# Performance work log

Measured on AMD Instinct MI355X. Metric: run time of the kernel, lower is better.

Reference implementation:

```python
import jax, jax.numpy as jnp
import numpy as np

N_WORD = 50000
N_DOC = 10000
E_WW = 800000
E_WD = 320000


def _sage(h_src, h_dst, src, dst, n_dst, W_self, W_neigh, b):
    # DGL SAGEConv('mean'): fc_self(h_dst) + fc_neigh(mean_{u in N(v)} h_u) + bias
    ones = jnp.ones((src.shape[0],), dtype=h_src.dtype)
    deg = jax.ops.segment_sum(ones, dst, num_segments=n_dst)            # [n_dst]
    agg = jax.ops.segment_sum(h_src[src], dst, num_segments=n_dst)      # [n_dst, d]
    mean = agg / jnp.maximum(deg, 1.0)[:, None]                          # zero for isolated
    return h_dst @ W_self + mean @ W_neigh + b


def _layer(xw, xd, edges, Ws, Wn, b):
    (ww_s, ww_d, wwr_s, wwr_d, wd_s, wd_d, wdr_s, wdr_d) = edges
    # relations targeting 'word': word2word, word2wordr, word2documentr
    h_ww = _sage(xw, xw, ww_s, ww_d, N_WORD, Ws[0], Wn[0], b[0])
    h_wwr = _sage(xw, xw, wwr_s, wwr_d, N_WORD, Ws[1], Wn[1], b[1])
    h_wdr = _sage(xd, xw, wdr_s, wdr_d, N_WORD, Ws[3], Wn[3], b[3])
    # relation targeting 'document': word2document
    h_wd = _sage(xw, xd, wd_s, wd_d, N_DOC, Ws[2], Wn[2], b[2])
    # HeteroGraphConv aggregate='stack' then torch.sum(dim=1) == sum over relations; then relu
    return jax.nn.relu(h_ww + h_wwr + h_wdr), jax.nn.relu(h_wd)


def setup_inputs() -> dict:
    key = jax.random.key(0)
    ks = jax.random.split(key, 20)
    d_in, d_h = 256, 128
    inp = {
        "x_word": jax.random.normal(ks[0], (N_WORD, d_in), jnp.float32),
        "x_doc": jax.random.normal(ks[1], (N_DOC, d_in), jnp.float32),
        "ww_src": jax.random.randint(ks[2], (E_WW,), 0, N_WORD, jnp.int32),
        "ww_dst": jax.random.randint(ks[3], (E_WW,), 0, N_WORD, jnp.int32),
        "wwr_src": jax.random.randint(ks[4], (E_WW,), 0, N_WORD, jnp.int32),
        "wwr_dst": jax.random.randint(ks[5], (E_WW,), 0, N_WORD, jnp.int32),
        "wd_src": jax.random.randint(ks[6], (E_WD,), 0, N_WORD, jnp.int32),
        "wd_dst": jax.random.randint(ks[7], (E_WD,), 0, N_DOC, jnp.int32),
        "wdr_src": jax.random.randint(ks[8], (E_WD,), 0, N_DOC, jnp.int32),
        "wdr_dst": jax.random.randint(ks[9], (E_WD,), 0, N_WORD, jnp.int32),
        "Wself1": jax.random.normal(ks[10], (4, d_in, d_h), jnp.float32) * (1.0 / np.sqrt(d_in)),
        "Wneigh1": jax.random.normal(ks[11], (4, d_in, d_h), jnp.float32) * (1.0 / np.sqrt(d_in)),
        "b1": jnp.zeros((4, d_h), jnp.float32),
        "Wself2": jax.random.normal(ks[12], (4, d_h, d_h), jnp.float32) * (1.0 / np.sqrt(d_h)),
        "Wneigh2": jax.random.normal(ks[13], (4, d_h, d_h), jnp.float32) * (1.0 / np.sqrt(d_h)),
        "b2": jnp.zeros((4, d_h), jnp.float32),
        "lin_w": jax.random.normal(ks[14], (1, d_h), jnp.float32) * (1.0 / np.sqrt(d_h)),
        "lin_b": jnp.ones((1,), jnp.float32),
    }
    return inp


def reference(x_word, x_doc, ww_src, ww_dst, wwr_src, wwr_dst, wd_src, wd_dst,
              wdr_src, wdr_dst, Wself1, Wneigh1, b1, Wself2, Wneigh2, b2, lin_w, lin_b):
    edges = (ww_src, ww_dst, wwr_src, wwr_dst, wd_src, wd_dst, wdr_src, wdr_dst)
    xw, xd = _layer(x_word, x_doc, edges, Wself1, Wneigh1, b1)
    xw, xd = _layer(xw, xd, edges, Wself2, Wneigh2, b2)
    out_w = jax.nn.sigmoid(xw @ lin_w.T + lin_b)  # [N_WORD, 1]
    out_d = jax.nn.sigmoid(xd @ lin_w.T + lin_b)  # [N_DOC, 1]
    return out_w, out_d
```

## Files before the change

### kernel.cpp

```cpp
#include <hip/hip_runtime.h>
#include <math.h>

#define N_WORD 50000
#define N_DOC  10000
#define E_WW   800000
#define E_WD   320000
#define D_IN   256
#define D_H    128

#define NPB    256
#define NBK_W  196
#define NBK_D  40
#define BKT    (3 * NBK_W + NBK_D)
#define EPB    8192
#define NBLK_WW 98
#define NBLK_WD 40
#define NBLK_TOT (2 * NBLK_WW + 2 * NBLK_WD)
#define PACK_BLKS 145

#define CAP_WW  4736
#define CAP_WDR 2176
#define CAP_WD  8960

#define WSTRIP ((N_WORD + 63) / 64)
#define DSTRIP ((N_DOC + 63) / 64)
#define NSTRIP (WSTRIP + DSTRIP)

typedef __attribute__((ext_vector_type(8))) short short8;
typedef __attribute__((ext_vector_type(4))) float f32x4;
typedef __attribute__((ext_vector_type(2))) float f32x2;

__device__ inline unsigned short f2bf(float f) {
  unsigned u = __float_as_uint(f);
  u = (u + 0x7fffu + ((u >> 16) & 1u)) >> 16;
  return (unsigned short)u;
}

__device__ inline float bflo(unsigned u) { return __uint_as_float(u << 16); }
__device__ inline float bfhi(unsigned u) { return __uint_as_float(u & 0xffff0000u); }

struct G6 { const short* B[6]; unsigned short* C[6]; };

#define BCH 16384

template <int ABF, int K>
__device__ void gemm_body(const void* __restrict__ Aw, const void* __restrict__ Ad,
                          const G6& g, int blk, short* __restrict__ Bs) {
  constexpr int KT = K >> 5;
  constexpr int NCH = KT / 4;
  int tid = threadIdx.x;
  int wid = tid >> 6, lane = tid & 63;
  const void* A; int M, row0, h0, h1;
  if (blk < WSTRIP) { A = Aw; M = N_WORD; row0 = blk << 6; h0 = 0; h1 = 4; }
  else { A = Ad; M = N_DOC; row0 = (blk - WSTRIP) << 6; h0 = 4; h1 = 6; }
  int r = lane & 15, quad = lane >> 4;
  int m0 = row0 + wid * 16;
  int mA = m0 + r; if (mA >= M) mA = M - 1;
  short8 afr[KT];
  if (ABF) {
    const short* ap = (const short*)A + (size_t)mA * K + quad * 8;
#pragma unroll
    for (int kt = 0; kt < KT; ++kt) afr[kt] = *(const short8*)(ap + kt * 32);
  } else {
    const float* ap = (const float*)A + (size_t)mA * K + quad * 8;
#pragma unroll
    for (int kt = 0; kt < KT; ++kt) {
      float4 a0 = *(const float4*)(ap + kt * 32);
      float4 a1 = *(const float4*)(ap + kt * 32 + 4);
      short8 v;
      v[0] = (short)f2bf(a0.x); v[1] = (short)f2bf(a0.y);
      v[2] = (short)f2bf(a0.z); v[3] = (short)f2bf(a0.w);
      v[4] = (short)f2bf(a1.x); v[5] = (short)f2bf(a1.y);
      v[6] = (short)f2bf(a1.z); v[7] = (short)f2bf(a1.w);
      afr[kt] = v;
    }
  }
  for (int h = h0; h < h1; ++h) {
    const short* Bp = g.B[h];
    f32x4 acc[8];
#pragma unroll
    for (int nt = 0; nt < 8; ++nt) acc[nt] = (f32x4){0.f, 0.f, 0.f, 0.f};
    for (int c = 0; c < NCH; ++c) {
      const short* src = Bp + (size_t)c * BCH;
#pragma unroll
      for (int i = 0; i < 8; ++i) {
        int o = (i * 256 + tid) * 8;
        *(short8*)(Bs + o) = *(const short8*)(src + o);
      }
      __syncthreads();
#pragma unroll
      for (int ktl = 0; ktl < 4; ++ktl) {
        const short* bbase = Bs + ktl * 4096 + lane * 8;
#pragma unroll
        for (int nt = 0; nt < 8; ++nt) {
          short8 bf = *(const short8*)(bbase + nt * 512);
          acc[nt] = __builtin_amdgcn_mfma_f32_16x16x32_bf16(afr[c * 4 + ktl], bf, acc[nt], 0, 0, 0);
        }
      }
      __syncthreads();
    }
    unsigned short* C = g.C[h];
#pragma unroll
    for (int nt = 0; nt < 8; ++nt)
#pragma unroll
      for (int rr = 0; rr < 4; ++rr) {
        int row = m0 + quad * 4 + rr;
        if (row < M) C[(size_t)row * 128 + nt * 16 + r] = f2bf(acc[nt][rr]);
      }
  }
}

__global__ __launch_bounds__(256, 2) void gemm2_kernel(
    const void* __restrict__ Aw, const void* __restrict__ Ad, G6 g) {
  __shared__ short Bs[BCH];
  gemm_body<1, 128>(Aw, Ad, g, blockIdx.x, Bs);
}

__global__ __launch_bounds__(256) void prep_kernel(
    const float* __restrict__ Ws1, const float* __restrict__ Wn1,
    const float* __restrict__ Ws2, const float* __restrict__ Wn2,
    short* __restrict__ Bp1, short* __restrict__ Bp2,
    const float* __restrict__ b1, const float* __restrict__ b2,
    float* __restrict__ bs1, float* __restrict__ bs2, int* __restrict__ bcnt,
    unsigned* __restrict__ zA, unsigned* __restrict__ zB,
    unsigned* __restrict__ zC, unsigned* __restrict__ zD) {
  int b = blockIdx.x;
  if (b == PACK_BLKS) {
    for (int i = threadIdx.x; i < BKT; i += 256) bcnt[i] = 0;
    if (threadIdx.x < 64) {
      zA[(size_t)N_WORD * 64 + threadIdx.x] = 0;
      zB[(size_t)N_WORD * 64 + threadIdx.x] = 0;
      zC[(size_t)N_WORD * 64 + threadIdx.x] = 0;
      zD[(size_t)N_DOC * 64 + threadIdx.x] = 0;
    }
    return;
  }
  int tid = b * 256 + threadIdx.x;
  const int L1T = 6 * 4096;
  const int L2T = 6 * 2048;
  if (tid >= L1T + L2T) {
    int t = tid - (L1T + L2T);
    if (t < 128) bs1[t] = b1[t] + b1[128 + t] + b1[384 + t];
    else if (t < 256) { int u = t - 128; bs2[u] = b2[u] + b2[128 + u] + b2[384 + u]; }
    return;
  }
  const float *src0, *src1 = nullptr, *src2 = nullptr;
  short* dstp;
  int kt, nt, lane;
  if (tid < L1T) {
    int mat = tid / 4096, rem = tid % 4096;
    kt = rem / 512; nt = (rem / 64) % 8; lane = rem % 64;
    const int W1 = 256 * 128;
    if (mat == 0) { src0 = Ws1; src1 = Ws1 + W1; src2 = Ws1 + 3 * W1; }
    else if (mat <= 4) src0 = Wn1 + (size_t)(mat - 1) * W1;
    else src0 = Ws1 + 2 * W1;
    dstp = Bp1 + (size_t)mat * W1 + ((size_t)(kt * 8 + nt) * 64 + lane) * 8;
  } else {
    int t2 = tid - L1T;
    int mat = t2 / 2048, rem = t2 % 2048;
    kt = rem / 512; nt = (rem / 64) % 8; lane = rem % 64;
    const int W2 = 128 * 128;
    if (mat == 0) { src0 = Ws2; src1 = Ws2 + W2; src2 = Ws2 + 3 * W2; }
    else if (mat <= 4) src0 = Wn2 + (size_t)(mat - 1) * W2;
    else src0 = Ws2 + 2 * W2;
    dstp = Bp2 + (size_t)mat * W2 + ((size_t)(kt * 8 + nt) * 64 + lane) * 8;
  }
  int n = nt * 16 + (lane & 15);
  int kb = kt * 32 + (lane >> 4) * 8;
  short8 v;
#pragma unroll
  for (int j = 0; j < 8; ++j) {
    float f = src0[(size_t)(kb + j) * 128 + n];
    if (src1) f += src1[(size_t)(kb + j) * 128 + n] + src2[(size_t)(kb + j) * 128 + n];
    v[j] = (short)f2bf(f);
  }
  *(short8*)dstp = v;
}

__device__ inline void rel_map(int b, const int* wwd, const int* wwrd, const int* wdrd,
                               const int* wdd, const int*& dst, int& E, int& gbase, int& lb) {
  if (b < NBLK_WW) { dst = wwd; E = E_WW; gbase = 0; lb = b; }
  else if (b < 2 * NBLK_WW) { dst = wwrd; E = E_WW; gbase = NBK_W; lb = b - NBLK_WW; }
  else if (b < 2 * NBLK_WW + NBLK_WD) { dst = wdrd; E = E_WD; gbase = 2 * NBK_W; lb = b - 2 * NBLK_WW; }
  else { dst = wdd; E = E_WD; gbase = 3 * NBK_W; lb = b - 2 * NBLK_WW - NBLK_WD; }
}

struct BinLDS {
  unsigned buf[EPB];
  int hist[NBK_W];
  int lofs[NBK_W];
  int gofs[NBK_W];
  int lcur[NBK_W];
  int sm[256];
};

union FusedLDS {
  BinLDS bin;
  short bs[BCH];
};

__global__ __launch_bounds__(256, 4) void bin_gemm1(
    const int* wws, const int* wwd, const int* wwrs, const int* wwrd,
    const int* wdrs, const int* wdrd, const int* wds, const int* wdd,
    int* bcnt, unsigned* st_ww, unsigned* st_wwr, unsigned* st_wdr, unsigned* st_wd,
    const float* __restrict__ Aw, const float* __restrict__ Ad, G6 g) {
  __shared__ FusedLDS U;
  int b = blockIdx.x;
  if (b >= NBLK_TOT) {
    gemm_body<0, 256>(Aw, Ad, g, b - NBLK_TOT, U.bs);
    return;
  }
  BinLDS& L = U.bin;
  const int* dst; int E, gbase, lb;
  rel_map(b, wwd, wwrd, wdrd, wdd, dst, E, gbase, lb);
  const int* src; unsigned* st; int cap;
  if (b < NBLK_WW) { src = wws; st = st_ww; cap = CAP_WW; }
  else if (b < 2 * NBLK_WW) { src = wwrs; st = st_wwr; cap = CAP_WW; }
  else if (b < 2 * NBLK_WW + NBLK_WD) { src = wdrs; st = st_wdr; cap = CAP_WDR; }
  else { src = wds; st = st_wd; cap = CAP_WD; }
  int tid = threadIdx.x;
  int e0 = lb * EPB;
  int ecnt = E - e0; if (ecnt > EPB) ecnt = EPB;
  if (tid < NBK_W) L.hist[tid] = 0;
  __syncthreads();
  int dcache[EPB / 256];
#pragma unroll
  for (int k = 0; k < EPB / 256; ++k) {
    int i = e0 + k * 256 + tid;
    int d = (i < E) ? dst[i] : -1;
    dcache[k] = d;
    if (d >= 0) atomicAdd(&L.hist[d >> 8], 1);
  }
  __syncthreads();
  {
    int v = (tid < NBK_W) ? L.hist[tid] : 0;
    L.sm[tid] = v;
    __syncthreads();
    for (int o = 1; o < 256; o <<= 1) {
      int add = (tid >= o) ? L.sm[tid - o] : 0;
      __syncthreads();
      L.sm[tid] += add;
      __syncthreads();
    }
    if (tid < NBK_W) {
      int ex = L.sm[tid] - v;
      L.lofs[tid] = ex;
      L.lcur[tid] = ex;
      int base = v ? atomicAdd(&bcnt[gbase + tid], v) : 0;
      L.gofs[tid] = (int)((size_t)tid * cap) + base - ex;
    }
  }
  __syncthreads();
#pragma unroll
  for (int k = 0; k < EPB / 256; ++k) {
    int d = dcache[k];
    if (d >= 0) {
      int i = e0 + k * 256 + tid;
      int bk = d >> 8;
      int p = atomicAdd(&L.lcur[bk], 1);
      L.buf[p] = ((unsigned)bk << 24) | ((unsigned)(d & 255) << 16) |
                 (unsigned)(src[i] & 0xFFFF);
    }
  }
  __syncthreads();
#pragma unroll
  for (int k = 0; k < EPB / 256; ++k) {
    int p = k * 256 + tid;
    if (p < ecnt) {
      unsigned e = L.buf[p];
      st[L.gofs[e >> 24] + p] = e & 0x00FFFFFFu;
    }
  }
}

struct CSRB {
  const unsigned *st_ww, *st_wwr, *st_wdr, *st_wd;
  unsigned short *c_ww, *c_wwr, *c_wdr, *c_wd;
  int *rp_ww, *rp_wwr, *rp_wdr, *rp_wd;
  const int* bcnt;
};

__global__ __launch_bounds__(256) void place_kernel(CSRB q) {
  __shared__ int cnt[256], off[256], sm[256];
  int g = blockIdx.x;
  const unsigned* st; unsigned short* csr; int* rp; int relFirst, relLast, n, cap, Etot;
  if (g < NBK_W)            { st = q.st_ww;  csr = q.c_ww;  rp = q.rp_ww;  relFirst = 0;         relLast = NBK_W - 1;     n = N_WORD; cap = CAP_WW;  Etot = E_WW; }
  else if (g < 2 * NBK_W)   { st = q.st_wwr; csr = q.c_wwr; rp = q.rp_wwr; relFirst = NBK_W;     relLast = 2 * NBK_W - 1; n = N_WORD; cap = CAP_WW;  Etot = E_WW; }
  else if (g < 3 * NBK_W)   { st = q.st_wdr; csr = q.c_wdr; rp = q.rp_wdr; relFirst = 2 * NBK_W; relLast = 3 * NBK_W - 1; n = N_WORD; cap = CAP_WDR; Etot = E_WD; }
  else                      { st = q.st_wd;  csr = q.c_wd;  rp = q.rp_wd;  relFirst = 3 * NBK_W; relLast = BKT - 1;       n = N_DOC;  cap = CAP_WD;  Etot = E_WD; }
  int cb = g - relFirst;
  int tid = threadIdx.x;
  int v = (tid < cb) ? q.bcnt[relFirst + tid] : 0;
  sm[tid] = v;
  __syncthreads();
  for (int o = 128; o > 0; o >>= 1) {
    if (tid < o) sm[tid] += sm[tid + o];
    __syncthreads();
  }
  int bstart = sm[0];
  if (g == relLast && tid == 0) rp[n] = Etot;
  __syncthreads();
  int node_base = cb << 8;
  int node_cnt = n - node_base; if (node_cnt > NPB) node_cnt = NPB;
  int ecnt = q.bcnt[g];
  const unsigned* w = st + (size_t)cb * cap;
  cnt[tid] = 0;
  __syncthreads();
  for (int j = tid; j < ecnt; j += 256) atomicAdd(&cnt[w[j] >> 16], 1);
  __syncthreads();
  int c = cnt[tid];
  sm[tid] = c;
  __syncthreads();
  for (int o = 1; o < 256; o <<= 1) {
    int add = (tid >= o) ? sm[tid - o] : 0;
    __syncthreads();
    sm[tid] += add;
    __syncthreads();
  }
  int ex = sm[tid] - c;
  off[tid] = ex;
  if (tid < node_cnt) rp[node_base + tid] = bstart + ex;
  __syncthreads();
  for (int j = tid; j < ecnt; j += 256) {
    unsigned e = w[j];
    int p = atomicAdd(&off[e >> 16], 1);
    csr[bstart + p] = (unsigned short)(e & 0xFFFFu);
  }
}

__device__ inline void accum_rel4(const uint4* __restrict__ Y,
                                  const unsigned short* __restrict__ csr,
                                  int beg, int end, int lane, int r, int g,
                                  int zrow, f32x2* __restrict__ f) {
  int deg = end - beg;
  if (deg <= 0) return;
  f32x2 a0 = {0.f, 0.f}, a1 = a0, a2 = a0, a3 = a0;
  for (int base = beg; base < end; base += 64) {
    int cnt = end - base; if (cnt > 64) cnt = 64;
    int ld = base + lane;
    int idx = (ld < end) ? (int)csr[ld] : zrow;
    for (int j = 0; j < cnt; j += 16) {
      uint4 u[4];
#pragma unroll
      for (int t = 0; t < 4; ++t) {
        int sv = __shfl(idx, j + (t << 2) + g, 64);
        u[t] = Y[(unsigned)((sv << 4) + r)];
      }
#pragma unroll
      for (int t = 0; t < 4; ++t) {
        a0 += (f32x2){bflo(u[t].x), bfhi(u[t].x)};
        a1 += (f32x2){bflo(u[t].y), bfhi(u[t].y)};
        a2 += (f32x2){bflo(u[t].z), bfhi(u[t].z)};
        a3 += (f32x2){bflo(u[t].w), bfhi(u[t].w)};
      }
    }
  }
  float inv = 1.0f / (float)deg;
  f[0] += a0 * inv; f[1] += a1 * inv; f[2] += a2 * inv; f[3] += a3 * inv;
}

__global__ __launch_bounds__(256) void gather_all(
    const unsigned* __restrict__ y_ww, const unsigned* __restrict__ y_wwr,
    const unsigned* __restrict__ y_wdr, const unsigned* __restrict__ y_wd,
    const unsigned short* __restrict__ c_ww, const unsigned short* __restrict__ c_wwr,
    const unsigned short* __restrict__ c_wdr, const unsigned short* __restrict__ c_wd,
    const int* __restrict__ r_ww, const int* __restrict__ r_wwr,
    const int* __restrict__ r_wdr, const int* __restrict__ r_wd,
    const unsigned* __restrict__ tW, const unsigned* __restrict__ tD,
    const float* __restrict__ bW, const float* __restrict__ bD,
    const float* __restrict__ lw, const float* __restrict__ lb,
    unsigned* __restrict__ oW16, unsigned* __restrict__ oD16,
    float* __restrict__ oF, int mode) {
  int gn = (blockIdx.x << 2) + (threadIdx.x >> 6);
  if (gn >= N_WORD + N_DOC) return;
  int lane = threadIdx.x & 63;
  int r = lane & 15, g = lane >> 4;
  f32x2 f[4];
#pragma unroll
  for (int i = 0; i < 4; ++i) f[i] = (f32x2){0.f, 0.f};
  bool isw = (gn < N_WORD);
  int node = isw ? gn : gn - N_WORD;
  if (isw) {
    accum_rel4((const uint4*)y_ww, c_ww, r_ww[node], r_ww[node + 1], lane, r, g, N_WORD, f);
    accum_rel4((const uint4*)y_wwr, c_wwr, r_wwr[node], r_wwr[node + 1], lane, r, g, N_WORD, f);
    accum_rel4((const uint4*)y_wdr, c_wdr, r_wdr[node], r_wdr[node + 1], lane, r, g, N_DOC, f);
  } else {
    accum_rel4((const uint4*)y_wd, c_wd, r_wd[node], r_wd[node + 1], lane, r, g, N_WORD, f);
  }
#pragma unroll
  for (int i = 0; i < 4; ++i) {
    f[i].x += __shfl_xor(f[i].x, 16, 64);
    f[i].y += __shfl_xor(f[i].y, 16, 64);
    f[i].x += __shfl_xor(f[i].x, 32, 64);
    f[i].y += __shfl_xor(f[i].y, 32, 64);
  }
  const unsigned* tS = isw ? tW : tD;
  uint4 tu = ((const uint4*)tS)[(unsigned)((node << 4) + r)];
  const float* bs = isw ? bW : bD;
  float4 bv0 = ((const float4*)bs)[2 * r];
  float4 bv1 = ((const float4*)bs)[2 * r + 1];
  f[0].x = fmaxf(f[0].x + bflo(tu.x) + bv0.x, 0.f);
  f[0].y = fmaxf(f[0].y + bfhi(tu.x) + bv0.y, 0.f);
  f[1].x = fmaxf(f[1].x + bflo(tu.y) + bv0.z, 0.f);
  f[1].y = fmaxf(f[1].y + bfhi(tu.y) + bv0.w, 0.f);
  f[2].x = fmaxf(f[2].x + bflo(tu.z) + bv1.x, 0.f);
  f[2].y = fmaxf(f[2].y + bfhi(tu.z) + bv1.y, 0.f);
  f[3].x = fmaxf(f[3].x + bflo(tu.w) + bv1.z, 0.f);
  f[3].y = fmaxf(f[3].y + bfhi(tu.w) + bv1.w, 0.f);
  if (mode == 1) {
    if (g == 0) {
      uint4 pk;
      pk.x = (unsigned)f2bf(f[0].x) | ((unsigned)f2bf(f[0].y) << 16);
      pk.y = (unsigned)f2bf(f[1].x) | ((unsigned)f2bf(f[1].y) << 16);
      pk.z = (unsigned)f2bf(f[2].x) | ((unsigned)f2bf(f[2].y) << 16);
      pk.w = (unsigned)f2bf(f[3].x) | ((unsigned)f2bf(f[3].y) << 16);
      unsigned* o = isw ? oW16 : oD16;
      ((uint4*)o)[(unsigned)((node << 4) + r)] = pk;
    }
  } else {
    float4 lv0 = ((const float4*)lw)[2 * r];
    float4 lv1 = ((const float4*)lw)[2 * r + 1];
    float s = f[0].x * lv0.x + f[0].y * lv0.y + f[1].x * lv0.z + f[1].y * lv0.w +
              f[2].x * lv1.x + f[2].y * lv1.y + f[3].x * lv1.z + f[3].y * lv1.w;
#pragma unroll
    for (int off = 8; off > 0; off >>= 1) s += __shfl_xor(s, off, 64);
    if (lane == 0) oF[isw ? node : N_WORD + node] = 1.0f / (1.0f + expf(-(s + lb[0])));
  }
}

extern "C" void kernel_launch(void* const* d_in, const int* in_sizes, int n_in,
                              void* d_out, int out_size, void* d_ws, size_t ws_size,
                              hipStream_t stream) {
  const float* xw      = (const float*)d_in[0];
  const float* xd      = (const float*)d_in[1];
  const int*   ww_src  = (const int*)d_in[2];
  const int*   ww_dst  = (const int*)d_in[3];
  const int*   wwr_src = (const int*)d_in[4];
  const int*   wwr_dst = (const int*)d_in[5];
  const int*   wd_src  = (const int*)d_in[6];
  const int*   wd_dst  = (const int*)d_in[7];
  const int*   wdr_src = (const int*)d_in[8];
  const int*   wdr_dst = (const int*)d_in[9];
  const float* Ws1     = (const float*)d_in[10];
  const float* Wn1     = (const float*)d_in[11];
  const float* b1      = (const float*)d_in[12];
  const float* Ws2     = (const float*)d_in[13];
  const float* Wn2     = (const float*)d_in[14];
  const float* b2      = (const float*)d_in[15];
  const float* lin_w   = (const float*)d_in[16];
  const float* lin_b   = (const float*)d_in[17];
  float* out = (float*)d_out;

  char* p = (char*)d_ws;
  auto alloc = [&](size_t nbytes) {
    char* r = p;
    p += (nbytes + 255) & ~(size_t)255;
    return r;
  };
  unsigned* twA  = (unsigned*)alloc((size_t)N_WORD * D_H * 2);
  unsigned* tdA  = (unsigned*)alloc((size_t)N_DOC * D_H * 2);
  unsigned* xw1B = (unsigned*)alloc((size_t)N_WORD * D_H * 2 + 256);
  unsigned* xd1B = (unsigned*)alloc((size_t)N_DOC * D_H * 2);
  unsigned* yB0 = (unsigned*)alloc((size_t)N_WORD * D_H * 2);
  unsigned* yB1 = (unsigned*)alloc(((size_t)NBK_W * CAP_WDR + (size_t)NBK_D * CAP_WD) * 4);
  unsigned* yB2 = (unsigned*)alloc((size_t)N_WORD * D_H * 2 + 256);
  unsigned* ydB = (unsigned*)alloc((size_t)N_DOC * D_H * 2 + 256);
  unsigned short* csr_ww  = (unsigned short*)alloc((size_t)E_WW * 2);
  unsigned short* csr_wwr = (unsigned short*)alloc((size_t)E_WW * 2);
  unsigned short* csr_wdr = (unsigned short*)alloc((size_t)E_WD * 2);
  unsigned short* csr_wd  = (unsigned short*)alloc((size_t)E_WD * 2);
  int* rp_ww  = (int*)alloc((size_t)(N_WORD + 1) * 4);
  int* rp_wwr = (int*)alloc((size_t)(N_WORD + 1) * 4);
  int* rp_wdr = (int*)alloc((size_t)(N_WORD + 1) * 4);
  int* rp_wd  = (int*)alloc((size_t)(N_DOC + 1) * 4);
  short* Bp1 = (short*)alloc((size_t)6 * 256 * 128 * 2);
  short* Bp2 = (short*)alloc((size_t)6 * 128 * 128 * 2);
  int* bcnt  = (int*)alloc((size_t)BKT * 4);
  float* bs1 = (float*)alloc(D_H * 4);
  float* bs2 = (float*)alloc(D_H * 4);
  unsigned* yBX = (unsigned*)alloc((size_t)N_WORD * D_H * 2 + 256);
  unsigned* st_ww  = yB0;
  unsigned* st_wwr = st_ww + (size_t)NBK_W * CAP_WW;
  unsigned* st_wdr = yB1;
  unsigned* st_wd  = st_wdr + (size_t)NBK_W * CAP_WDR;

  const int W1 = 256 * 128;
  const int W2 = 128 * 128;

  prep_kernel<<<PACK_BLKS + 1, 256, 0, stream>>>(
      Ws1, Wn1, Ws2, Wn2, Bp1, Bp2, b1, b2, bs1, bs2, bcnt,
      yB2, xw1B, yBX, ydB);

  G6 g1;
  g1.B[0] = Bp1 + 0 * W1; g1.C[0] = (unsigned short*)twA;
  g1.B[1] = Bp1 + 1 * W1; g1.C[1] = (unsigned short*)yB2;
  g1.B[2] = Bp1 + 2 * W1; g1.C[2] = (unsigned short*)xw1B;
  g1.B[3] = Bp1 + 3 * W1; g1.C[3] = (unsigned short*)yBX;
  g1.B[4] = Bp1 + 5 * W1; g1.C[4] = (unsigned short*)tdA;
  g1.B[5] = Bp1 + 4 * W1; g1.C[5] = (unsigned short*)ydB;
  bin_gemm1<<<NBLK_TOT + NSTRIP, 256, 0, stream>>>(
      ww_src, ww_dst, wwr_src, wwr_dst, wdr_src, wdr_dst, wd_src, wd_dst,
      bcnt, st_ww, st_wwr, st_wdr, st_wd, xw, xd, g1);

  CSRB q;
  q.st_ww = st_ww; q.st_wwr = st_wwr; q.st_wdr = st_wdr; q.st_wd = st_wd;
  q.c_ww = csr_ww; q.c_wwr = csr_wwr; q.c_wdr = csr_wdr; q.c_wd = csr_wd;
  q.rp_ww = rp_ww; q.rp_wwr = rp_wwr; q.rp_wdr = rp_wdr; q.rp_wd = rp_wd;
  q.bcnt = bcnt;
  place_kernel<<<BKT, 256, 0, stream>>>(q);

  gather_all<<<(N_WORD + N_DOC + 3) / 4, 256, 0, stream>>>(
      yB2, xw1B, ydB, yBX, csr_ww, csr_wwr, csr_wdr, csr_wd,
      rp_ww, rp_wwr, rp_wdr, rp_wd, twA, tdA, bs1, b1 + 256,
      lin_w, lin_b, yB0, xd1B, nullptr, 1);

  G6 g2;
  g2.B[0] = Bp2 + 0 * W2; g2.C[0] = (unsigned short*)twA;
  g2.B[1] = Bp2 + 1 * W2; g2.C[1] = (unsigned short*)yB2;
  g2.B[2] = Bp2 + 2 * W2; g2.C[2] = (unsigned short*)xw1B;
  g2.B[3] = Bp2 + 3 * W2; g2.C[3] = (unsigned short*)yBX;
  g2.B[4] = Bp2 + 5 * W2; g2.C[4] = (unsigned short*)tdA;
  g2.B[5] = Bp2 + 4 * W2; g2.C[5] = (unsigned short*)ydB;
  gemm2_kernel<<<NSTRIP, 256, 0, stream>>>(yB0, xd1B, g2);

  gather_all<<<(N_WORD + N_DOC + 3) / 4, 256, 0, stream>>>(
      yB2, xw1B, ydB, yBX, csr_ww, csr_wwr, csr_wdr, csr_wd,
      rp_ww, rp_wwr, rp_wdr, rp_wd, twA, tdA, bs2, b2 + 256,
      lin_w, lin_b, nullptr, nullptr, out, 2);
}
```

Baseline: 367.2 us.

## Reorder layer 2 as aggregate-then-transform and fuse final linear into GEMM

Layer 2 used to transform node features first (GEMM) and then gather the transformed rows. It now gathers neighbour means of the raw 128-wide layer-1 outputs for each relation, then runs one fused GEMM that concatenates self and mean operands along K. That GEMM applies bias, ReLU, the final linear projection and the sigmoid in registers, so the bf16 C buffers for layer 2 are never written out. Because d_in equals d_out in layer 2, the gather moves the same number of bytes, but the mean tensors are rounded to bf16 before the GEMM, which changes numerics slightly.

```diff
diff --git a/kernel.cpp b/kernel.cpp
--- a/kernel.cpp
+++ b/kernel.cpp
@@ -42,6 +42,7 @@
 struct G6 { const short* B[6]; unsigned short* C[6]; };
 
 #define BCH 16384
+#define W2SZ 16384
 
 template <int ABF, int K>
 __device__ void gemm_body(const void* __restrict__ Aw, const void* __restrict__ Ad,
@@ -110,10 +111,90 @@
   }
 }
 
-__global__ __launch_bounds__(256, 2) void gemm2_kernel(
-    const void* __restrict__ Aw, const void* __restrict__ Ad, G6 g) {
-  __shared__ short Bs[BCH];
-  gemm_body<1, 128>(Aw, Ad, g, blockIdx.x, Bs);
+template <int NS>
+__device__ void gemm2_fused(const unsigned* A0, const unsigned* A1,
+                            const unsigned* A2, const unsigned* A3,
+                            const short* B0, const short* B1,
+                            const short* B2, const short* B3,
+                            int M, int row0, const float* __restrict__ bias, int ob,
+                            const float* __restrict__ lw, const float* __restrict__ lb,
+                            float* __restrict__ out, short* __restrict__ Bs) {
+  const unsigned* As[4] = {A0, A1, A2, A3};
+  const short* Bm[4] = {B0, B1, B2, B3};
+  int tid = threadIdx.x;
+  int wid = tid >> 6, lane = tid & 63;
+  int r = lane & 15, quad = lane >> 4;
+  int m0 = row0 + wid * 16;
+  int mA = m0 + r; if (mA >= M) mA = M - 1;
+  short8 afr[NS][4];
+#pragma unroll
+  for (int s = 0; s < NS; ++s) {
+    const short* ap = (const short*)As[s] + (size_t)mA * 128 + quad * 8;
+#pragma unroll
+    for (int kt = 0; kt < 4; ++kt) afr[s][kt] = *(const short8*)(ap + kt * 32);
+  }
+  f32x4 acc[8];
+#pragma unroll
+  for (int nt = 0; nt < 8; ++nt) acc[nt] = (f32x4){0.f, 0.f, 0.f, 0.f};
+#pragma unroll
+  for (int s = 0; s < NS; ++s) {
+    const short* src = Bm[s];
+#pragma unroll
+    for (int i = 0; i < 8; ++i) {
+      int o = (i * 256 + tid) * 8;
+      *(short8*)(Bs + o) = *(const short8*)(src + o);
+    }
+    __syncthreads();
+#pragma unroll
+    for (int ktl = 0; ktl < 4; ++ktl) {
+      const short* bbase = Bs + ktl * 4096 + lane * 8;
+#pragma unroll
+      for (int nt = 0; nt < 8; ++nt) {
+        short8 bf = *(const short8*)(bbase + nt * 512);
+        acc[nt] = __builtin_amdgcn_mfma_f32_16x16x32_bf16(afr[s][ktl], bf, acc[nt], 0, 0, 0);
+      }
+    }
+    __syncthreads();
+  }
+  float bsv[8], lwv[8];
+#pragma unroll
+  for (int nt = 0; nt < 8; ++nt) { bsv[nt] = bias[nt * 16 + r]; lwv[nt] = lw[nt * 16 + r]; }
+  float lbv = lb[0];
+#pragma unroll
+  for (int rr = 0; rr < 4; ++rr) {
+    float p = 0.f;
+#pragma unroll
+    for (int nt = 0; nt < 8; ++nt) {
+      float v = acc[nt][rr] + bsv[nt];
+      v = fmaxf(v, 0.f);
+      p += v * lwv[nt];
+    }
+    p += __shfl_xor(p, 1, 64);
+    p += __shfl_xor(p, 2, 64);
+    p += __shfl_xor(p, 4, 64);
+    p += __shfl_xor(p, 8, 64);
+    int row = m0 + quad * 4 + rr;
+    if (r == 0 && row < M) out[ob + row] = 1.0f / (1.0f + expf(-(p + lbv)));
+  }
+}
+
+__global__ __launch_bounds__(256, 2) void gemm2f_kernel(
+    const unsigned* __restrict__ x1w, const unsigned* __restrict__ x1d,
+    const unsigned* __restrict__ mww, const unsigned* __restrict__ mwwr,
+    const unsigned* __restrict__ mwdr, const unsigned* __restrict__ mwd,
+    const short* __restrict__ Bp2, const float* __restrict__ bsW,
+    const float* __restrict__ bsD, const float* __restrict__ lw,
+    const float* __restrict__ lb, float* __restrict__ out) {
+  __shared__ short Bs[W2SZ];
+  int blk = blockIdx.x;
+  if (blk < WSTRIP)
+    gemm2_fused<4>(x1w, mww, mwwr, mwdr,
+                   Bp2, Bp2 + W2SZ, Bp2 + 2 * W2SZ, Bp2 + 4 * W2SZ,
+                   N_WORD, blk << 6, bsW, 0, lw, lb, out, Bs);
+  else
+    gemm2_fused<2>(x1d, mwd, nullptr, nullptr,
+                   Bp2 + 5 * W2SZ, Bp2 + 3 * W2SZ, nullptr, nullptr,
+                   N_DOC, (blk - WSTRIP) << 6, bsD, N_WORD, lw, lb, out, Bs);
 }
 
 __global__ __launch_bounds__(256) void prep_kernel(
@@ -123,7 +204,8 @@
     const float* __restrict__ b1, const float* __restrict__ b2,
     float* __restrict__ bs1, float* __restrict__ bs2, int* __restrict__ bcnt,
     unsigned* __restrict__ zA, unsigned* __restrict__ zB,
-    unsigned* __restrict__ zC, unsigned* __restrict__ zD) {
+    unsigned* __restrict__ zC, unsigned* __restrict__ zD,
+    unsigned* __restrict__ zE, unsigned* __restrict__ zF) {
   int b = blockIdx.x;
   if (b == PACK_BLKS) {
     for (int i = threadIdx.x; i < BKT; i += 256) bcnt[i] = 0;
@@ -132,6 +214,8 @@
       zB[(size_t)N_WORD * 64 + threadIdx.x] = 0;
       zC[(size_t)N_WORD * 64 + threadIdx.x] = 0;
       zD[(size_t)N_DOC * 64 + threadIdx.x] = 0;
+      zE[(size_t)N_WORD * 64 + threadIdx.x] = 0;
+      zF[(size_t)N_DOC * 64 + threadIdx.x] = 0;
     }
     return;
   }
@@ -159,11 +243,10 @@
     int t2 = tid - L1T;
     int mat = t2 / 2048, rem = t2 % 2048;
     kt = rem / 512; nt = (rem / 64) % 8; lane = rem % 64;
-    const int W2 = 128 * 128;
-    if (mat == 0) { src0 = Ws2; src1 = Ws2 + W2; src2 = Ws2 + 3 * W2; }
-    else if (mat <= 4) src0 = Wn2 + (size_t)(mat - 1) * W2;
-    else src0 = Ws2 + 2 * W2;
-    dstp = Bp2 + (size_t)mat * W2 + ((size_t)(kt * 8 + nt) * 64 + lane) * 8;
+    if (mat == 0) { src0 = Ws2; src1 = Ws2 + W2SZ; src2 = Ws2 + 3 * W2SZ; }
+    else if (mat <= 4) src0 = Wn2 + (size_t)(mat - 1) * W2SZ;
+    else src0 = Ws2 + 2 * W2SZ;
+    dstp = Bp2 + (size_t)mat * W2SZ + ((size_t)(kt * 8 + nt) * 64 + lane) * 8;
   }
   int n = nt * 16 + (lane & 15);
   int kb = kt * 32 + (lane >> 4) * 8;
@@ -368,9 +451,7 @@
     const int* __restrict__ r_wdr, const int* __restrict__ r_wd,
     const unsigned* __restrict__ tW, const unsigned* __restrict__ tD,
     const float* __restrict__ bW, const float* __restrict__ bD,
-    const float* __restrict__ lw, const float* __restrict__ lb,
-    unsigned* __restrict__ oW16, unsigned* __restrict__ oD16,
-    float* __restrict__ oF, int mode) {
+    unsigned* __restrict__ oW16, unsigned* __restrict__ oD16) {
   int gn = (blockIdx.x << 2) + (threadIdx.x >> 6);
   if (gn >= N_WORD + N_DOC) return;
   int lane = threadIdx.x & 63;
@@ -407,24 +488,69 @@
   f[2].y = fmaxf(f[2].y + bfhi(tu.z) + bv1.y, 0.f);
   f[3].x = fmaxf(f[3].x + bflo(tu.w) + bv1.z, 0.f);
   f[3].y = fmaxf(f[3].y + bfhi(tu.w) + bv1.w, 0.f);
-  if (mode == 1) {
-    if (g == 0) {
-      uint4 pk;
-      pk.x = (unsigned)f2bf(f[0].x) | ((unsigned)f2bf(f[0].y) << 16);
-      pk.y = (unsigned)f2bf(f[1].x) | ((unsigned)f2bf(f[1].y) << 16);
-      pk.z = (unsigned)f2bf(f[2].x) | ((unsigned)f2bf(f[2].y) << 16);
-      pk.w = (unsigned)f2bf(f[3].x) | ((unsigned)f2bf(f[3].y) << 16);
-      unsigned* o = isw ? oW16 : oD16;
-      ((uint4*)o)[(unsigned)((node << 4) + r)] = pk;
-    }
+  if (g == 0) {
+    uint4 pk;
+    pk.x = (unsigned)f2bf(f[0].x) | ((unsigned)f2bf(f[0].y) << 16);
+    pk.y = (unsigned)f2bf(f[1].x) | ((unsigned)f2bf(f[1].y) << 16);
+    pk.z = (unsigned)f2bf(f[2].x) | ((unsigned)f2bf(f[2].y) << 16);
+    pk.w = (unsigned)f2bf(f[3].x) | ((unsigned)f2bf(f[3].y) << 16);
+    unsigned* o = isw ? oW16 : oD16;
+    ((uint4*)o)[(unsigned)((node << 4) + r)] = pk;
+  }
+}
+
+__device__ inline void mean_write(int node, int lane, int r, int g,
+                                  f32x2* __restrict__ A, unsigned* __restrict__ mT) {
+#pragma unroll
+  for (int i = 0; i < 4; ++i) {
+    A[i].x += __shfl_xor(A[i].x, 16, 64);
+    A[i].y += __shfl_xor(A[i].y, 16, 64);
+    A[i].x += __shfl_xor(A[i].x, 32, 64);
+    A[i].y += __shfl_xor(A[i].y, 32, 64);
+  }
+  if (g == 0) {
+    uint4 pk;
+    pk.x = (unsigned)f2bf(A[0].x) | ((unsigned)f2bf(A[0].y) << 16);
+    pk.y = (unsigned)f2bf(A[1].x) | ((unsigned)f2bf(A[1].y) << 16);
+    pk.z = (unsigned)f2bf(A[2].x) | ((unsigned)f2bf(A[2].y) << 16);
+    pk.w = (unsigned)f2bf(A[3].x) | ((unsigned)f2bf(A[3].y) << 16);
+    ((uint4*)mT)[(unsigned)((node << 4) + r)] = pk;
+  }
+}
+
+__global__ __launch_bounds__(256) void gather_mean(
+    const unsigned* __restrict__ yW, const unsigned* __restrict__ yD,
+    const unsigned short* __restrict__ c_ww, const unsigned short* __restrict__ c_wwr,
+    const unsigned short* __restrict__ c_wdr, const unsigned short* __restrict__ c_wd,
+    const int* __restrict__ r_ww, const int* __restrict__ r_wwr,
+    const int* __restrict__ r_wdr, const int* __restrict__ r_wd,
+    unsigned* __restrict__ mWW, unsigned* __restrict__ mWWR,
+    unsigned* __restrict__ mWDR, unsigned* __restrict__ mWD) {
+  int gn = (blockIdx.x << 2) + (threadIdx.x >> 6);
+  if (gn >= N_WORD + N_DOC) return;
+  int lane = threadIdx.x & 63;
+  int r = lane & 15, g = lane >> 4;
+  bool isw = (gn < N_WORD);
+  int node = isw ? gn : gn - N_WORD;
+  f32x2 A[4];
+  if (isw) {
+#pragma unroll
+    for (int i = 0; i < 4; ++i) A[i] = (f32x2){0.f, 0.f};
+    accum_rel4((const uint4*)yW, c_ww, r_ww[node], r_ww[node + 1], lane, r, g, N_WORD, A);
+    mean_write(node, lane, r, g, A, mWW);
+#pragma unroll
+    for (int i = 0; i < 4; ++i) A[i] = (f32x2){0.f, 0.f};
+    accum_rel4((const uint4*)yW, c_wwr, r_wwr[node], r_wwr[node + 1], lane, r, g, N_WORD, A);
+    mean_write(node, lane, r, g, A, mWWR);
+#pragma unroll
+    for (int i = 0; i < 4; ++i) A[i] = (f32x2){0.f, 0.f};
+    accum_rel4((const uint4*)yD, c_wdr, r_wdr[node], r_wdr[node + 1], lane, r, g, N_DOC, A);
+    mean_write(node, lane, r, g, A, mWDR);
   } else {
-    float4 lv0 = ((const float4*)lw)[2 * r];
-    float4 lv1 = ((const float4*)lw)[2 * r + 1];
-    float s = f[0].x * lv0.x + f[0].y * lv0.y + f[1].x * lv0.z + f[1].y * lv0.w +
-              f[2].x * lv1.x + f[2].y * lv1.y + f[3].x * lv1.z + f[3].y * lv1.w;
-#pragma unroll
-    for (int off = 8; off > 0; off >>= 1) s += __shfl_xor(s, off, 64);
-    if (lane == 0) oF[isw ? node : N_WORD + node] = 1.0f / (1.0f + expf(-(s + lb[0])));
+#pragma unroll
+    for (int i = 0; i < 4; ++i) A[i] = (f32x2){0.f, 0.f};
+    accum_rel4((const uint4*)yW, c_wd, r_wd[node], r_wd[node + 1], lane, r, g, N_WORD, A);
+    mean_write(node, lane, r, g, A, mWD);
   }
 }
 
@@ -460,8 +586,8 @@
   unsigned* twA  = (unsigned*)alloc((size_t)N_WORD * D_H * 2);
   unsigned* tdA  = (unsigned*)alloc((size_t)N_DOC * D_H * 2);
   unsigned* xw1B = (unsigned*)alloc((size_t)N_WORD * D_H * 2 + 256);
-  unsigned* xd1B = (unsigned*)alloc((size_t)N_DOC * D_H * 2);
-  unsigned* yB0 = (unsigned*)alloc((size_t)N_WORD * D_H * 2);
+  unsigned* xd1B = (unsigned*)alloc((size_t)N_DOC * D_H * 2 + 256);
+  unsigned* yB0 = (unsigned*)alloc((size_t)N_WORD * D_H * 2 + 256);
   unsigned* yB1 = (unsigned*)alloc(((size_t)NBK_W * CAP_WDR + (size_t)NBK_D * CAP_WD) * 4);
   unsigned* yB2 = (unsigned*)alloc((size_t)N_WORD * D_H * 2 + 256);
   unsigned* ydB = (unsigned*)alloc((size_t)N_DOC * D_H * 2 + 256);
@@ -485,11 +611,10 @@
   unsigned* st_wd  = st_wdr + (size_t)NBK_W * CAP_WDR;
 
   const int W1 = 256 * 128;
-  const int W2 = 128 * 128;
 
   prep_kernel<<<PACK_BLKS + 1, 256, 0, stream>>>(
       Ws1, Wn1, Ws2, Wn2, Bp1, Bp2, b1, b2, bs1, bs2, bcnt,
-      yB2, xw1B, yBX, ydB);
+      yB2, xw1B, yBX, ydB, yB0, xd1B);
 
   G6 g1;
   g1.B[0] = Bp1 + 0 * W1; g1.C[0] = (unsigned short*)twA;
@@ -512,19 +637,14 @@
   gather_all<<<(N_WORD + N_DOC + 3) / 4, 256, 0, stream>>>(
       yB2, xw1B, ydB, yBX, csr_ww, csr_wwr, csr_wdr, csr_wd,
       rp_ww, rp_wwr, rp_wdr, rp_wd, twA, tdA, bs1, b1 + 256,
-      lin_w, lin_b, yB0, xd1B, nullptr, 1);
-
-  G6 g2;
-  g2.B[0] = Bp2 + 0 * W2; g2.C[0] = (unsigned short*)twA;
-  g2.B[1] = Bp2 + 1 * W2; g2.C[1] = (unsigned short*)yB2;
-  g2.B[2] = Bp2 + 2 * W2; g2.C[2] = (unsigned short*)xw1B;
-  g2.B[3] = Bp2 + 3 * W2; g2.C[3] = (unsigned short*)yBX;
-  g2.B[4] = Bp2 + 5 * W2; g2.C[4] = (unsigned short*)tdA;
-  g2.B[5] = Bp2 + 4 * W2; g2.C[5] = (unsigned short*)ydB;
-  gemm2_kernel<<<NSTRIP, 256, 0, stream>>>(yB0, xd1B, g2);
-
-  gather_all<<<(N_WORD + N_DOC + 3) / 4, 256, 0, stream>>>(
-      yB2, xw1B, ydB, yBX, csr_ww, csr_wwr, csr_wdr, csr_wd,
-      rp_ww, rp_wwr, rp_wdr, rp_wd, twA, tdA, bs2, b2 + 256,
-      lin_w, lin_b, nullptr, nullptr, out, 2);
-}
+      yB0, xd1B);
+
+  gather_mean<<<(N_WORD + N_DOC + 3) / 4, 256, 0, stream>>>(
+      yB0, xd1B, csr_ww, csr_wwr, csr_wdr, csr_wd,
+      rp_ww, rp_wwr, rp_wdr, rp_wd,
+      yB2 , xw1B , yBX , ydB );
+
+  gemm2f_kernel<<<NSTRIP, 256, 0, stream>>>(
+      yB0, xd1B, yB2, xw1B, yBX, ydB, Bp2, bs2, b2 + 256,
+      lin_w, lin_b, out);
+}
```

Result: faster. 359.7 us, median of 2 (-2.0%).
